# Optimization experiments

Hardware: AMD Instinct MI355X
Metric: run time of the kernel (lower is better)

The kernel has to match this reference:

```python
import jax, jax.numpy as jnp
import numpy as np

N_HEADS = 8
N_GROUPS = 32
EPS = 1e-5


def setup_inputs() -> dict:
    key = jax.random.key(0)
    ks = jax.random.split(key, 3)
    b, c, h, w = 8, 512, 32, 32
    x = jax.random.normal(ks[0], (b, c, h, w), dtype=jnp.float32)
    gamma = jnp.ones((c,), jnp.float32)
    beta = jnp.zeros((c,), jnp.float32)
    w_qkv = jax.random.normal(ks[1], (3 * c, c), jnp.float32) * (1.0 / np.sqrt(c))
    b_qkv = jnp.zeros((3 * c,), jnp.float32)
    w_proj = jax.random.normal(ks[2], (c, c), jnp.float32) * (1.0 / np.sqrt(c))
    b_proj = jnp.zeros((c,), jnp.float32)
    return {"x": x, "gamma": gamma, "beta": beta, "w_qkv": w_qkv,
            "b_qkv": b_qkv, "w_proj": w_proj, "b_proj": b_proj}


def _group_norm(x, gamma, beta):
    # x: [b, c, T]; GroupNorm over (c//G, T) per group, computed in fp32
    b, c, t = x.shape
    xg = x.reshape(b, N_GROUPS, c // N_GROUPS, t).astype(jnp.float32)
    mean = xg.mean(axis=(2, 3), keepdims=True)
    var = xg.var(axis=(2, 3), keepdims=True)
    xg = (xg - mean) * jax.lax.rsqrt(var + EPS)
    xn = xg.reshape(b, c, t).astype(x.dtype)
    return xn * gamma[None, :, None] + beta[None, :, None]


def reference(x, gamma, beta, w_qkv, b_qkv, w_proj, b_proj):
    b, c, *spatial = x.shape
    t = int(np.prod(spatial))
    xf = x.reshape(b, c, t)
    h = _group_norm(xf, gamma, beta)
    # 1x1 conv == channel matmul
    qkv = jnp.einsum('oc,bct->bot', w_qkv, h) + b_qkv[None, :, None]  # [b, 3c, t]
    ch = c // N_HEADS
    qkv = qkv.reshape(b * N_HEADS, 3 * ch, t)
    q, k, v = qkv[:, :ch], qkv[:, ch:2 * ch], qkv[:, 2 * ch:]
    scale = 1.0 / np.sqrt(np.sqrt(ch))
    weight = jnp.einsum('bct,bcs->bts', q * scale, k * scale)
    weight = jax.nn.softmax(weight.astype(jnp.float32), axis=-1).astype(weight.dtype)
    a = jnp.einsum('bts,bcs->bct', weight, v)  # [b*H, ch, t]
    a = a.reshape(b, c, t)
    h = jnp.einsum('oc,bct->bot', w_proj, a) + b_proj[None, :, None]
    return (xf + h).reshape(b, c, *spatial)
```

## Files before the change

### kernel.cpp

```cpp
#include <hip/hip_runtime.h>
#include <hip/hip_bf16.h>
#include <math.h>

#define BATCH 8
#define CDIM 512
#define TDIM 1024
#define NHD 8

typedef __attribute__((ext_vector_type(8))) _Float16 f16x8;
typedef __attribute__((ext_vector_type(4))) float floatx4;

#define QSCALE 0.18033688011112042f
#define EBIAS 6.0f

static __device__ __forceinline__ unsigned short f2h(float f) {
    _Float16 h = (_Float16)f;
    return *reinterpret_cast<unsigned short*>(&h);
}
static __device__ __forceinline__ void async_load16(const unsigned short* gsrc,
                                                    unsigned short* ldst) {
    __builtin_amdgcn_global_load_lds(
        (const __attribute__((address_space(1))) void*)gsrc,
        (__attribute__((address_space(3))) void*)ldst, 16, 0, 0);
}

__global__ __launch_bounds__(256) void prep_kernel(
    const float* __restrict__ x, const float* __restrict__ gamma,
    const float* __restrict__ beta, const float* __restrict__ w_qkv,
    const float* __restrict__ w_proj, unsigned short* __restrict__ h_t,
    unsigned short* __restrict__ wq, unsigned short* __restrict__ wp) {
    int tid = threadIdx.x;
    if (blockIdx.x >= 256) {
        int i = (blockIdx.x - 256) * 256 + tid;
        const int nA = 1536 * 512 / 4;
        const float* s;
        unsigned short* d;
        int j;
        if (i < nA) { s = w_qkv; d = wq; j = i; }
        else        { s = w_proj; d = wp; j = i - nA; }
        float4 v = ((const float4*)s)[j];
        ushort4 o;
        o.x = f2h(v.x); o.y = f2h(v.y); o.z = f2h(v.z); o.w = f2h(v.w);
        ((ushort4*)d)[j] = o;
        return;
    }
    int bg = blockIdx.x;
    int b = bg >> 5, g = bg & 31;
    const float* xp = x + ((size_t)(b * CDIM + g * 16)) * TDIM;

    float s = 0.f, ss = 0.f;
    for (int r = 0; r < 16; ++r) {
        float4 v = ((const float4*)xp)[r * 256 + tid];
        s  += v.x + v.y + v.z + v.w;
        ss += v.x * v.x + v.y * v.y + v.z * v.z + v.w * v.w;
    }
    for (int off = 32; off > 0; off >>= 1) {
        s  += __shfl_down(s, off, 64);
        ss += __shfl_down(ss, off, 64);
    }
    __shared__ float rs[4], rss[4], stat[2];
    int wave = tid >> 6;
    if ((tid & 63) == 0) { rs[wave] = s; rss[wave] = ss; }
    __syncthreads();
    if (tid == 0) {
        float S  = rs[0] + rs[1] + rs[2] + rs[3];
        float SS = rss[0] + rss[1] + rss[2] + rss[3];
        float mean = S * (1.f / 16384.f);
        float var  = SS * (1.f / 16384.f) - mean * mean;
        stat[0] = mean;
        stat[1] = rsqrtf(var + 1e-5f);
    }
    __syncthreads();
    float mean = stat[0], rstd = stat[1];

    int cpair = tid & 7, trow = tid >> 3;
    int c0 = g * 16 + cpair * 2;
    float g0 = gamma[c0] * rstd,  g1 = gamma[c0 + 1] * rstd;
    float b0 = beta[c0] - mean * g0, b1 = beta[c0 + 1] - mean * g1;
    const float* x0 = x + ((size_t)(b * CDIM + c0)) * TDIM;
    const float* x1 = x0 + TDIM;
    unsigned int* hp = (unsigned int*)h_t + (size_t)b * TDIM * 256 + g * 8 + cpair;
    for (int p = 0; p < 32; ++p) {
        int t = p * 32 + trow;
        float v0 = x0[t] * g0 + b0;
        float v1 = x1[t] * g1 + b1;
        hp[(size_t)t * 256] = (unsigned)f2h(v0) | ((unsigned)f2h(v1) << 16);
    }
}

template <int BM>
__global__ __launch_bounds__(256) void mfma_gemm(
    const unsigned short* __restrict__ Wb,
    const unsigned short* __restrict__ Xt,
    const float* __restrict__ bias,
    int K, int mode,
    unsigned short* __restrict__ q_t,
    unsigned short* __restrict__ k_t,
    unsigned short* __restrict__ v,
    const float* __restrict__ resid,
    float* __restrict__ outp) {
    constexpr int AF = BM / 32;
    __shared__ __align__(16) unsigned short As[BM * 64];
    __shared__ __align__(16) unsigned short Bs[128 * 64];

    int tid = threadIdx.x;
    int n0 = blockIdx.x * 128, m0 = blockIdx.y * BM, bb = blockIdx.z;
    const unsigned short* Xp = Xt + (size_t)bb * TDIM * K;

    int lane = tid & 63, w = tid >> 6;
    int l15 = lane & 15, quad = lane >> 4;
    int wm = w >> 1, wn = w & 1;

    const unsigned short* aSrc[AF];
    unsigned short* aDst[AF];
#pragma unroll
    for (int c = 0; c < AF; ++c) {
        int slot = w * 64 * AF + c * 64 + lane;
        int row = slot >> 3, g = (slot & 7) ^ (row & 7);
        aSrc[c] = Wb + (size_t)(m0 + row) * K + g * 8;
        aDst[c] = &As[(w * 64 * AF + c * 64) * 8];
    }
    const unsigned short* bSrc[4];
    unsigned short* bDst[4];
#pragma unroll
    for (int c = 0; c < 4; ++c) {
        int slot = w * 256 + c * 64 + lane;
        int row = slot >> 3, g = (slot & 7) ^ (row & 7);
        bSrc[c] = Xp + (size_t)(n0 + row) * K + g * 8;
        bDst[c] = &Bs[(w * 256 + c * 64) * 8];
    }

    floatx4 acc[AF][4];
#pragma unroll
    for (int i = 0; i < AF; ++i)
#pragma unroll
        for (int j = 0; j < 4; ++j) acc[i][j] = (floatx4){0.f, 0.f, 0.f, 0.f};

    for (int k0 = 0; k0 < K; k0 += 64) {
#pragma unroll
        for (int c = 0; c < AF; ++c) async_load16(aSrc[c] + k0, aDst[c]);
#pragma unroll
        for (int c = 0; c < 4; ++c) async_load16(bSrc[c] + k0, bDst[c]);
        __syncthreads();
#pragma unroll
        for (int kc = 0; kc < 2; ++kc) {
            f16x8 af[AF], bfr[4];
#pragma unroll
            for (int mi = 0; mi < AF; ++mi) {
                int row = wm * (BM / 2) + mi * 16 + l15;
                af[mi] = *(const f16x8*)&As[row * 64 + ((kc * 4 + quad) ^ (row & 7)) * 8];
            }
#pragma unroll
            for (int ni = 0; ni < 4; ++ni) {
                int row = wn * 64 + ni * 16 + l15;
                bfr[ni] = *(const f16x8*)&Bs[row * 64 + ((kc * 4 + quad) ^ (row & 7)) * 8];
            }
#pragma unroll
            for (int mi = 0; mi < AF; ++mi)
#pragma unroll
                for (int ni = 0; ni < 4; ++ni)
                    acc[mi][ni] = __builtin_amdgcn_mfma_f32_16x16x32_f16(
                        af[mi], bfr[ni], acc[mi][ni], 0, 0, 0);
        }
        __syncthreads();
    }

    if (mode == 0) {
        if constexpr (BM == 128) {
            int chunk = (m0 >> 6) + wm;
            int hd = chunk / 3, part = chunk % 3;
            int bh = bb * NHD + hd;
            __syncthreads();
            if (part < 2) {
                float scale = part == 0 ? QSCALE : 1.0f;
                unsigned short* dst = part == 0 ? q_t : k_t;
#pragma unroll
                for (int mi = 0; mi < 4; ++mi) {
                    int mBase = chunk * 64 + mi * 16 + quad * 4;
                    int cB = mBase & 63;
#pragma unroll
                    for (int ni = 0; ni < 4; ++ni) {
                        floatx4 a = acc[mi][ni];
                        int n = n0 + wn * 64 + ni * 16 + l15;
                        ushort4 pk;
                        pk.x = f2h((a[0] + bias[mBase + 0]) * scale);
                        pk.y = f2h((a[1] + bias[mBase + 1]) * scale);
                        pk.z = f2h((a[2] + bias[mBase + 2]) * scale);
                        pk.w = f2h((a[3] + bias[mBase + 3]) * scale);
                        *(ushort4*)&dst[((size_t)bh * TDIM + n) * 64 + cB] = pk;
                    }
                }
            } else {
                unsigned short* scr = (w < 2) ? &As[w * 4096] : &Bs[(w - 2) * 4096];
#pragma unroll
                for (int mi = 0; mi < 4; ++mi)
#pragma unroll
                    for (int ni = 0; ni < 4; ++ni) {
                        floatx4 a = acc[mi][ni];
#pragma unroll
                        for (int r = 0; r < 4; ++r) {
                            int c = mi * 16 + quad * 4 + r;
                            int j = ni * 16 + l15;
                            int seg = j >> 3;
                            scr[c * 64 + ((seg ^ (c & 7)) * 8) + (j & 7)] =
                                f2h(a[r] + bias[chunk * 64 + c]);
                        }
                    }
                int rr = lane >> 3, seg = lane & 7;
#pragma unroll
                for (int it = 0; it < 8; ++it) {
                    int c = it * 8 + rr;
                    uint4 val = *(const uint4*)&scr[c * 64 + ((seg ^ (c & 7)) * 8)];
                    *(uint4*)&v[((size_t)bh * 64 + c) * TDIM + n0 + wn * 64 + seg * 8] = val;
                }
            }
        }
    } else {
#pragma unroll
        for (int mi = 0; mi < AF; ++mi) {
            int mBase = m0 + wm * (BM / 2) + mi * 16 + quad * 4;
#pragma unroll
            for (int ni = 0; ni < 4; ++ni) {
                floatx4 a = acc[mi][ni];
                int n = n0 + wn * 64 + ni * 16 + l15;
                size_t base = ((size_t)bb * CDIM + mBase) * TDIM + n;
#pragma unroll
                for (int r = 0; r < 4; ++r)
                    outp[base + (size_t)r * TDIM] =
                        a[r] + bias[mBase + r] + resid[base + (size_t)r * TDIM];
            }
        }
    }
}

__global__ __launch_bounds__(128, 2) void attn_kernel(
    const unsigned short* __restrict__ q_t,
    const unsigned short* __restrict__ k_t,
    const unsigned short* __restrict__ v,
    unsigned short* __restrict__ a_t) {
    __shared__ __align__(16) unsigned short Kb[2][64 * 64];
    __shared__ __align__(16) unsigned short Vb[2][64 * 64];

    int tid = threadIdx.x;
    int bh = blockIdx.x;
    int q0 = blockIdx.y * 64;
    int lane = tid & 63, w = tid >> 6;
    int l15 = lane & 15, quad = lane >> 4;
    int l7 = l15 & 7;

    const unsigned short* Qp = q_t + (size_t)bh * TDIM * 64;
    const unsigned short* Kp = k_t + (size_t)bh * TDIM * 64;
    const unsigned short* Vp = v + (size_t)bh * 64 * TDIM;

    int kofs[4], vofs[4];
    unsigned short* kdst[4];
    unsigned short* vdst[4];
#pragma unroll
    for (int c = 0; c < 4; ++c) {
        int s_ = w * 256 + c * 64 + lane;
        int m = s_ >> 3, gs = s_ & 7, g = gs ^ (m & 7);
        int mi = m >> 4, qq = (m >> 2) & 3, rr = m & 3;
        int pm = (mi & 1) * 32 + qq * 8 + (mi >> 1) * 4 + rr;
        kofs[c] = pm * 64 + g * 8;
        vofs[c] = m * TDIM + g * 8;
        kdst[c] = &Kb[0][(w * 256 + c * 64) * 8];
        vdst[c] = &Vb[0][(w * 256 + c * 64) * 8];
    }
    const int bufstep = 64 * 64;

#pragma unroll
    for (int c = 0; c < 4; ++c) {
        async_load16(Kp + kofs[c], kdst[c]);
        async_load16(Vp + vofs[c], vdst[c]);
    }

    f16x8 qf[2][2];
#pragma unroll
    for (int f = 0; f < 2; ++f)
#pragma unroll
        for (int ch = 0; ch < 2; ++ch)
            qf[f][ch] = *(const f16x8*)(Qp + (size_t)(q0 + w * 32 + f * 16 + l15) * 64 +
                                        (ch * 4 + quad) * 8);

    floatx4 o_acc[4][2];
#pragma unroll
    for (int i = 0; i < 4; ++i)
#pragma unroll
        for (int j = 0; j < 2; ++j) o_acc[i][j] = (floatx4){0.f, 0.f, 0.f, 0.f};
    float l_acc[2] = {0.f, 0.f};

    __syncthreads();

    for (int it = 0; it < 16; ++it) {
        int cur = it & 1;
        if (it < 15) {
            int s0n = (it + 1) * 64;
#pragma unroll
            for (int c = 0; c < 4; ++c) {
                async_load16(Kp + (size_t)s0n * 64 + kofs[c], kdst[c] + (cur ^ 1) * bufstep);
                async_load16(Vp + s0n + vofs[c], vdst[c] + (cur ^ 1) * bufstep);
            }
        }
        f16x8 kf[4][2];
#pragma unroll
        for (int mi = 0; mi < 4; ++mi)
#pragma unroll
            for (int ch = 0; ch < 2; ++ch)
                kf[mi][ch] = *(const f16x8*)&Kb[cur][(mi * 16 + l15) * 64 +
                                                    ((ch * 4 + quad) ^ l7) * 8];

        floatx4 sT[2][4];
#pragma unroll
        for (int f = 0; f < 2; ++f)
#pragma unroll
            for (int mi = 0; mi < 4; ++mi) {
                floatx4 z = (floatx4){0.f, 0.f, 0.f, 0.f};
                z = __builtin_amdgcn_mfma_f32_16x16x32_f16(kf[mi][0], qf[f][0], z, 0, 0, 0);
                z = __builtin_amdgcn_mfma_f32_16x16x32_f16(kf[mi][1], qf[f][1], z, 0, 0, 0);
                sT[f][mi] = z;
            }

        f16x8 vf[4][2];
#pragma unroll
        for (int ci = 0; ci < 4; ++ci)
#pragma unroll
            for (int ch = 0; ch < 2; ++ch)
                vf[ci][ch] = *(const f16x8*)&Vb[cur][(ci * 16 + l15) * 64 +
                                                    ((ch * 4 + quad) ^ l7) * 8];

        f16x8 pf[2][2];
#pragma unroll
        for (int f = 0; f < 2; ++f) {
            float sum = 0.f;
#pragma unroll
            for (int mi = 0; mi < 4; ++mi)
#pragma unroll
                for (int r = 0; r < 4; ++r) {
                    float p = __builtin_amdgcn_exp2f(sT[f][mi][r] - EBIAS);
                    sT[f][mi][r] = p;
                    sum += p;
                }
            l_acc[f] += sum;
#pragma unroll
            for (int kb = 0; kb < 2; ++kb) {
                pf[f][kb][0] = (_Float16)sT[f][kb][0];
                pf[f][kb][1] = (_Float16)sT[f][kb][1];
                pf[f][kb][2] = (_Float16)sT[f][kb][2];
                pf[f][kb][3] = (_Float16)sT[f][kb][3];
                pf[f][kb][4] = (_Float16)sT[f][kb + 2][0];
                pf[f][kb][5] = (_Float16)sT[f][kb + 2][1];
                pf[f][kb][6] = (_Float16)sT[f][kb + 2][2];
                pf[f][kb][7] = (_Float16)sT[f][kb + 2][3];
            }
        }

#pragma unroll
        for (int ci = 0; ci < 4; ++ci)
#pragma unroll
            for (int f = 0; f < 2; ++f)
#pragma unroll
                for (int kb = 0; kb < 2; ++kb)
                    o_acc[ci][f] = __builtin_amdgcn_mfma_f32_16x16x32_f16(
                        vf[ci][kb], pf[f][kb], o_acc[ci][f], 0, 0, 0);
        __syncthreads();
    }

    int b = bh >> 3, hd = bh & 7;
#pragma unroll
    for (int f = 0; f < 2; ++f) {
        float l = l_acc[f];
        l += __shfl_xor(l, 16);
        l += __shfl_xor(l, 32);
        float linv = 1.f / l;
        int t = q0 + w * 32 + f * 16 + l15;
        size_t rowb = ((size_t)b * TDIM + t) * CDIM + hd * 64 + quad * 4;
#pragma unroll
        for (int ci = 0; ci < 4; ++ci) {
            ushort4 pk;
            pk.x = f2h(o_acc[ci][f][0] * linv);
            pk.y = f2h(o_acc[ci][f][1] * linv);
            pk.z = f2h(o_acc[ci][f][2] * linv);
            pk.w = f2h(o_acc[ci][f][3] * linv);
            *(ushort4*)&a_t[rowb + ci * 16] = pk;
        }
    }
}

extern "C" void kernel_launch(void* const* d_in, const int* in_sizes, int n_in,
                              void* d_out, int out_size, void* d_ws, size_t ws_size,
                              hipStream_t stream) {
    (void)in_sizes; (void)n_in; (void)out_size; (void)ws_size;
    const float* x      = (const float*)d_in[0];
    const float* gamma  = (const float*)d_in[1];
    const float* beta   = (const float*)d_in[2];
    const float* w_qkv  = (const float*)d_in[3];
    const float* b_qkv  = (const float*)d_in[4];
    const float* w_proj = (const float*)d_in[5];
    const float* b_proj = (const float*)d_in[6];
    float* out = (float*)d_out;

    unsigned short* wq  = (unsigned short*)d_ws;
    unsigned short* wp  = wq + 1536 * 512;
    unsigned short* h_t = wp + 512 * 512;
    unsigned short* q_t = h_t + (size_t)BATCH * TDIM * CDIM;
    unsigned short* k_t = q_t + (size_t)64 * TDIM * 64;
    unsigned short* vv  = k_t + (size_t)64 * TDIM * 64;
    unsigned short* a_t = vv + (size_t)64 * TDIM * 64;

    prep_kernel<<<1280, 256, 0, stream>>>(x, gamma, beta, w_qkv, w_proj, h_t, wq, wp);

    mfma_gemm<128><<<dim3(8, 12, BATCH), 256, 0, stream>>>(
        wq, h_t, b_qkv, 512, 0, q_t, k_t, vv, nullptr, nullptr);

    attn_kernel<<<dim3(64, 16), 128, 0, stream>>>(q_t, k_t, vv, a_t);

    mfma_gemm<64><<<dim3(8, 8, BATCH), 256, 0, stream>>>(
        wp, a_t, b_proj, 512, 1, nullptr, nullptr, nullptr, x, out);
}
```

Baseline: 155.0 us.

## Overlap next K-tile async LDS load with second half of MFMA compute

Restructures the GEMM main loop so the first tile is prefetched before the loop. After both k-halves of fragments are read into registers, the next tile's global-to-LDS loads are issued before the second half of the MFMAs runs, so load latency hides behind compute. This uses a single LDS buffer but more registers, since both fragment sets are held at once, which could lower occupancy.

```diff
diff --git a/kernel.cpp b/kernel.cpp
--- a/kernel.cpp
+++ b/kernel.cpp
@@ -136,33 +136,58 @@
 #pragma unroll
         for (int j = 0; j < 4; ++j) acc[i][j] = (floatx4){0.f, 0.f, 0.f, 0.f};
 
+#pragma unroll
+    for (int c = 0; c < AF; ++c) async_load16(aSrc[c], aDst[c]);
+#pragma unroll
+    for (int c = 0; c < 4; ++c) async_load16(bSrc[c], bDst[c]);
+
     for (int k0 = 0; k0 < K; k0 += 64) {
-#pragma unroll
-        for (int c = 0; c < AF; ++c) async_load16(aSrc[c] + k0, aDst[c]);
-#pragma unroll
-        for (int c = 0; c < 4; ++c) async_load16(bSrc[c] + k0, bDst[c]);
         __syncthreads();
-#pragma unroll
-        for (int kc = 0; kc < 2; ++kc) {
-            f16x8 af[AF], bfr[4];
-#pragma unroll
-            for (int mi = 0; mi < AF; ++mi) {
-                int row = wm * (BM / 2) + mi * 16 + l15;
-                af[mi] = *(const f16x8*)&As[row * 64 + ((kc * 4 + quad) ^ (row & 7)) * 8];
-            }
-#pragma unroll
-            for (int ni = 0; ni < 4; ++ni) {
-                int row = wn * 64 + ni * 16 + l15;
-                bfr[ni] = *(const f16x8*)&Bs[row * 64 + ((kc * 4 + quad) ^ (row & 7)) * 8];
-            }
-#pragma unroll
-            for (int mi = 0; mi < AF; ++mi)
-#pragma unroll
-                for (int ni = 0; ni < 4; ++ni)
-                    acc[mi][ni] = __builtin_amdgcn_mfma_f32_16x16x32_f16(
-                        af[mi], bfr[ni], acc[mi][ni], 0, 0, 0);
+
+        f16x8 af0[AF], bf0[4];
+#pragma unroll
+        for (int mi = 0; mi < AF; ++mi) {
+            int row = wm * (BM / 2) + mi * 16 + l15;
+            af0[mi] = *(const f16x8*)&As[row * 64 + (quad ^ (row & 7)) * 8];
+        }
+#pragma unroll
+        for (int ni = 0; ni < 4; ++ni) {
+            int row = wn * 64 + ni * 16 + l15;
+            bf0[ni] = *(const f16x8*)&Bs[row * 64 + (quad ^ (row & 7)) * 8];
+        }
+#pragma unroll
+        for (int mi = 0; mi < AF; ++mi)
+#pragma unroll
+            for (int ni = 0; ni < 4; ++ni)
+                acc[mi][ni] = __builtin_amdgcn_mfma_f32_16x16x32_f16(
+                    af0[mi], bf0[ni], acc[mi][ni], 0, 0, 0);
+
+        f16x8 af1[AF], bf1[4];
+#pragma unroll
+        for (int mi = 0; mi < AF; ++mi) {
+            int row = wm * (BM / 2) + mi * 16 + l15;
+            af1[mi] = *(const f16x8*)&As[row * 64 + ((4 + quad) ^ (row & 7)) * 8];
+        }
+#pragma unroll
+        for (int ni = 0; ni < 4; ++ni) {
+            int row = wn * 64 + ni * 16 + l15;
+            bf1[ni] = *(const f16x8*)&Bs[row * 64 + ((4 + quad) ^ (row & 7)) * 8];
         }
         __syncthreads();
+
+        if (k0 + 64 < K) {
+#pragma unroll
+            for (int c = 0; c < AF; ++c) async_load16(aSrc[c] + k0 + 64, aDst[c]);
+#pragma unroll
+            for (int c = 0; c < 4; ++c) async_load16(bSrc[c] + k0 + 64, bDst[c]);
+        }
+
+#pragma unroll
+        for (int mi = 0; mi < AF; ++mi)
+#pragma unroll
+            for (int ni = 0; ni < 4; ++ni)
+                acc[mi][ni] = __builtin_amdgcn_mfma_f32_16x16x32_f16(
+                    af1[mi], bf1[ni], acc[mi][ni], 0, 0, 0);
     }
 
     if (mode == 0) {
```

Result: no change. 153.8 us (-0.8%).
